# Kernel tuning notes

Hardware: AMD Instinct MI355X
Metric: run time of the kernel (lower is better)

## Reference

```python
import jax, jax.numpy as jnp
import numpy as np

N_NODES = 100000
N_EDGES = 1600000
F_IN, HID = 256, 256
HID_OUT = HID // 2  # last SAGE layer output


def _glorot(key, shape):
    fan_in, fan_out = shape[1], shape[0]
    lim = (6.0 / (fan_in + fan_out)) ** 0.5
    return jax.random.uniform(key, shape, jnp.float32, -lim, lim)


def setup_inputs() -> dict:
    key = jax.random.key(0)
    ks = jax.random.split(key, 12)
    x = jax.random.normal(ks[0], (N_NODES, F_IN), jnp.float32)
    edge_index = jax.random.randint(ks[1], (2, N_EDGES), 0, N_NODES, jnp.int64)
    # SAGEConv params: lin_l (on aggregated neighbors, has bias), lin_r (on root)
    dims = [(F_IN, HID), (HID, HID), (HID, HID_OUT)]
    inp = {"x": x, "edge_index": edge_index}
    for i, (din, dout) in enumerate(dims):
        inp[f"Wl{i}"] = _glorot(ks[2 + 3 * i], (dout, din))
        inp[f"Wr{i}"] = _glorot(ks[3 + 3 * i], (dout, din))
        inp[f"b{i}"] = jnp.zeros((dout,), jnp.float32)
    inp["Wc"] = _glorot(ks[11], (1, HID_OUT))
    inp["bc"] = jnp.zeros((1,), jnp.float32)
    return inp


def _sage_conv(x, src, dst, Wl, Wr, b):
    # mean aggregation of source features at destination nodes
    msg_sum = jax.ops.segment_sum(x[src], dst, num_segments=N_NODES)  # [N, d]
    deg = jax.ops.segment_sum(jnp.ones((src.shape[0], 1), x.dtype), dst,
                              num_segments=N_NODES)  # [N, 1]
    agg = msg_sum / jnp.maximum(deg, 1.0)
    return agg @ Wl.T + x @ Wr.T + b


def reference(x, edge_index, Wl0, Wr0, b0, Wl1, Wr1, b1, Wl2, Wr2, b2, Wc, bc):
    src, dst = edge_index[0], edge_index[1]
    layers = [(Wl0, Wr0, b0), (Wl1, Wr1, b1), (Wl2, Wr2, b2)]
    h = x
    for i, (Wl, Wr, b) in enumerate(layers):
        h = _sage_conv(h, src, dst, Wl, Wr, b)
        if i < len(layers) - 1:
            h = jax.nn.relu(h)  # dropout is identity in eval mode
    return jax.nn.sigmoid(h @ Wc.T + bc)  # [N, 1]
```

## Files before the change

### kernel.cpp

```cpp
#include <hip/hip_runtime.h>
#include <math.h>

#define N_NODES 100000
#define N_PAD   100352
#define N_EDGES 1600000
#define DIN 256

#define NB 782
#define NC 256
#define CHUNK 6250
#define MT_N (NB * NC)
#define MT_PAD 200448

typedef unsigned short u16;
typedef unsigned char u8;
typedef unsigned int u32;
typedef __attribute__((ext_vector_type(8))) short bf16x8;
typedef __attribute__((ext_vector_type(8))) unsigned short us8;
typedef __attribute__((ext_vector_type(4))) float f32x4;
typedef __attribute__((ext_vector_type(2))) float f32x2;

__device__ __forceinline__ float b2f(u16 u) {
    union { unsigned int i; float f; } c; c.i = ((unsigned int)u) << 16; return c.f;
}
__device__ __forceinline__ u16 f2b(float f) {
    union { float f; unsigned int i; } c; c.f = f;
    unsigned int x = c.i;
    return (u16)((x + 0x7fffu + ((x >> 16) & 1u)) >> 16);
}
__device__ __forceinline__ u8 f32_to_fp8(float v) {
    return (u8)(__builtin_amdgcn_cvt_pk_fp8_f32(v, 0.0f, 0, false) & 0xff);
}
__device__ __forceinline__ void accum16(float* a, uint4 v) {
    unsigned int w[4] = { v.x, v.y, v.z, v.w };
    #pragma unroll
    for (int q = 0; q < 4; ++q) {
        f32x2 lo = __builtin_amdgcn_cvt_pk_f32_fp8(w[q], false);
        f32x2 hi = __builtin_amdgcn_cvt_pk_f32_fp8(w[q], true);
        a[q * 4 + 0] += lo[0]; a[q * 4 + 1] += lo[1];
        a[q * 4 + 2] += hi[0]; a[q * 4 + 3] += hi[1];
    }
}
__device__ __forceinline__ void accum8(float* a, uint2 v) {
    unsigned int w[2] = { v.x, v.y };
    #pragma unroll
    for (int q = 0; q < 2; ++q) {
        f32x2 lo = __builtin_amdgcn_cvt_pk_f32_fp8(w[q], false);
        f32x2 hi = __builtin_amdgcn_cvt_pk_f32_fp8(w[q], true);
        a[q * 4 + 0] += lo[0]; a[q * 4 + 1] += lo[1];
        a[q * 4 + 2] += hi[0]; a[q * 4 + 3] += hi[1];
    }
}

__device__ __forceinline__ void gload_lds16(const u16* g, u16* lds_base) {
    __builtin_amdgcn_global_load_lds(
        (const __attribute__((address_space(1))) void*)g,
        (__attribute__((address_space(3))) void*)lds_base, 16, 0, 0);
}

__global__ void cvt_kernel(const float* __restrict__ in, u16* __restrict__ outb,
                           u8* __restrict__ out8, int n4) {
    int i = blockIdx.x * blockDim.x + threadIdx.x;
    if (i < n4) {
        float4 v = ((const float4*)in)[i];
        ushort4 o;
        o.x = f2b(v.x); o.y = f2b(v.y); o.z = f2b(v.z); o.w = f2b(v.w);
        ((ushort4*)outb)[i] = o;
        u32 r = __builtin_amdgcn_cvt_pk_fp8_f32(v.x, v.y, 0, false);
        r = __builtin_amdgcn_cvt_pk_fp8_f32(v.z, v.w, r, true);
        ((u32*)out8)[i] = r;
    }
}

__global__ void cvtw_kernel(const float* __restrict__ Wl0, const float* __restrict__ Wr0,
                            const float* __restrict__ Wl1, const float* __restrict__ Wr1,
                            const float* __restrict__ Wl2, const float* __restrict__ Wr2,
                            u16* __restrict__ wl0, u16* __restrict__ wr0,
                            u16* __restrict__ wl1, u16* __restrict__ wr1,
                            u16* __restrict__ wl2, u16* __restrict__ wr2) {
    int b = blockIdx.x;
    const float* s; u16* d; int i;
    if (b < 64)       { s = Wl0; d = wl0; i = b * 256 + threadIdx.x; }
    else if (b < 128) { s = Wr0; d = wr0; i = (b - 64) * 256 + threadIdx.x; }
    else if (b < 192) { s = Wl1; d = wl1; i = (b - 128) * 256 + threadIdx.x; }
    else if (b < 256) { s = Wr1; d = wr1; i = (b - 192) * 256 + threadIdx.x; }
    else if (b < 288) { s = Wl2; d = wl2; i = (b - 256) * 256 + threadIdx.x; }
    else              { s = Wr2; d = wr2; i = (b - 288) * 256 + threadIdx.x; }
    float4 v = ((const float4*)s)[i];
    ushort4 o;
    o.x = f2b(v.x); o.y = f2b(v.y); o.z = f2b(v.z); o.w = f2b(v.w);
    ((ushort4*)d)[i] = o;
}

__launch_bounds__(256)
__global__ void p1_hist(const int* __restrict__ dst, int* __restrict__ MT) {
    __shared__ int bins[NB];
    const int c = blockIdx.x, tid = threadIdx.x;
    for (int b = tid; b < NB; b += 256) bins[b] = 0;
    __syncthreads();
    const int e0 = c * CHUNK;
    for (int e = e0 + tid; e < e0 + CHUNK; e += 256)
        atomicAdd(&bins[dst[e] >> 7], 1);
    __syncthreads();
    for (int b = tid; b < NB; b += 256) MT[b * NC + c] = bins[b];
}

__global__ void scan1_kernel(const int* __restrict__ in, int* __restrict__ excl,
                             int* __restrict__ blocksums, int n) {
    __shared__ int s[256];
    int tid = threadIdx.x;
    int i = blockIdx.x * 256 + tid;
    int v = (i < n) ? in[i] : 0;
    s[tid] = v;
    __syncthreads();
    for (int off = 1; off < 256; off <<= 1) {
        int t = (tid >= off) ? s[tid - off] : 0;
        __syncthreads();
        s[tid] += t;
        __syncthreads();
    }
    if (i < n) excl[i] = s[tid] - v;
    if (tid == 255) blocksums[blockIdx.x] = s[255];
}

__global__ void scan_carry_kernel(int* __restrict__ bsums, int nb) {
    __shared__ int s[256];
    int tid = threadIdx.x;
    int carry = 0;
    for (int base = 0; base < nb; base += 256) {
        int i = base + tid;
        int v = (i < nb) ? bsums[i] : 0;
        s[tid] = v;
        __syncthreads();
        for (int off = 1; off < 256; off <<= 1) {
            int t = (tid >= off) ? s[tid - off] : 0;
            __syncthreads();
            s[tid] += t;
            __syncthreads();
        }
        int incl = s[tid];
        int tot = s[255];
        if (i < nb) bsums[i] = incl - v + carry;
        carry += tot;
        __syncthreads();
    }
}

__global__ void scan3_kernel(int* __restrict__ excl, const int* __restrict__ blocksums, int n) {
    int i = blockIdx.x * 256 + threadIdx.x;
    if (i < n) excl[i] += blocksums[blockIdx.x];
}

__launch_bounds__(256)
__global__ void p2_partition(const int* __restrict__ src, const int* __restrict__ dst,
                             const int* __restrict__ scanMT, u32* __restrict__ csr_tmp) {
    __shared__ int cur[NB];
    const int c = blockIdx.x, tid = threadIdx.x;
    for (int b = tid; b < NB; b += 256) cur[b] = scanMT[b * NC + c];
    __syncthreads();
    const int e0 = c * CHUNK;
    for (int e = e0 + tid; e < e0 + CHUNK; e += 256) {
        int d = dst[e];
        int pos = atomicAdd(&cur[d >> 7], 1);
        csr_tmp[pos] = ((u32)(d & 127) << 25) | (u32)src[e];
    }
}

__launch_bounds__(256)
__global__ void p3_csr(const int* __restrict__ scanMT, const u32* __restrict__ csr_tmp,
                       int* __restrict__ csr, int* __restrict__ rowptr,
                       int* __restrict__ rowend, float* __restrict__ rinv) {
    __shared__ int cnt[128];
    __shared__ int excl[128];
    __shared__ int cur[128];
    const int b = blockIdx.x, tid = threadIdx.x;
    const int beg = scanMT[b * NC];
    const int end = (b == NB - 1) ? N_EDGES : scanMT[(b + 1) * NC];
    if (tid < 128) cnt[tid] = 0;
    __syncthreads();
    for (int e = beg + tid; e < end; e += 256)
        atomicAdd(&cnt[csr_tmp[e] >> 25], 1);
    __syncthreads();
    if (tid == 0) {
        int run = 0;
        for (int i = 0; i < 128; ++i) { excl[i] = run; run += cnt[i]; }
    }
    __syncthreads();
    if (tid < 128) cur[tid] = beg + excl[tid];
    __syncthreads();
    for (int e = beg + tid; e < end; e += 256) {
        u32 v = csr_tmp[e];
        int pos = atomicAdd(&cur[v >> 25], 1);
        csr[pos] = (int)(v & 0x1FFFFFFu);
    }
    if (tid < 128) {
        int node = b * 128 + tid;
        if (node < N_NODES) {
            int rp = beg + excl[tid];
            rowptr[node] = rp;
            rowend[node] = rp + cnt[tid];
            rinv[node]   = 1.0f / (float)max(cnt[tid], 1);
        }
    }
}

__launch_bounds__(256)
__global__ void agg_kernel(const int* __restrict__ rowptr, const int* __restrict__ rowend,
                           const int* __restrict__ csr_src, const float* __restrict__ rinv,
                           const u8* __restrict__ h8, u16* __restrict__ agg) {
    int node = blockIdx.x * 16 + (threadIdx.x >> 4);
    int lane = threadIdx.x & 15;
    if (node >= N_NODES) return;
    int beg = rowptr[node];
    int end = rowend[node];
    const u8* hl = h8 + lane * 16;
    float a[16] = {};
    int p = beg;
    for (; p + 3 < end; p += 4) {
        int s0 = csr_src[p], s1 = csr_src[p + 1], s2 = csr_src[p + 2], s3 = csr_src[p + 3];
        uint4 v0 = *(const uint4*)(hl + (size_t)s0 * 256);
        uint4 v1 = *(const uint4*)(hl + (size_t)s1 * 256);
        uint4 v2 = *(const uint4*)(hl + (size_t)s2 * 256);
        uint4 v3 = *(const uint4*)(hl + (size_t)s3 * 256);
        accum16(a, v0); accum16(a, v1); accum16(a, v2); accum16(a, v3);
    }
    for (; p < end; ++p) {
        uint4 v0 = *(const uint4*)(hl + (size_t)csr_src[p] * 256);
        accum16(a, v0);
    }
    float r = rinv[node];
    us8 o0, o1;
    #pragma unroll
    for (int j = 0; j < 8; ++j) { o0[j] = f2b(a[j] * r); o1[j] = f2b(a[8 + j] * r); }
    u16* d = agg + (size_t)node * DIN + lane * 16;
    *(us8*)d = o0;
    *(us8*)(d + 8) = o1;
}

template <int MODE>
__launch_bounds__(256)
__global__ void sage_gemm(const u16* __restrict__ A0, const u16* __restrict__ A1,
                          const u16* __restrict__ B0w, const u16* __restrict__ B1w,
                          const float* __restrict__ bias, void* __restrict__ out0,
                          void* __restrict__ out1, u8* __restrict__ out8,
                          int dout, int do_relu) {
    __shared__ u16 sA[2][128 * 32];
    __shared__ u16 sB[2][128 * 32];

    const int t    = threadIdx.x;
    const int row0 = blockIdx.x * 128;
    const int col0 = (MODE == 0) ? blockIdx.y * 128 : 0;
    const int w    = t >> 6, lane = t & 63;
    const int wr   = w >> 1, wc = w & 1;
    const int lr   = lane & 15, lg = lane >> 4;
    const int srow = lane >> 2;
    const int sblk = (lane & 3) ^ (srow & 3);
    const u16* Bsrc_all = (MODE == 1 && blockIdx.y == 1) ? B1w : B0w;

    f32x4 acc[4][4] = {};
    const int NT = (MODE == 0) ? 16 : 8;

    auto stage = [&](int buf, int tk) {
        const int kt = tk * 32;
        const u16* Asrc = (MODE == 0 && kt >= 256) ? A1 : A0;
        const u16* Bsrc = (MODE == 0) ? ((kt >= 256) ? B1w : B0w) : Bsrc_all;
        const int  kb   = (MODE == 0 && kt >= 256) ? kt - 256 : kt;
        #pragma unroll
        for (int i = 0; i < 2; ++i) {
            int row = w * 32 + i * 16 + srow;
            gload_lds16(Asrc + (size_t)(row0 + row) * DIN + kb + sblk * 8,
                        &sA[buf][w * 1024 + i * 512]);
            gload_lds16(Bsrc + (size_t)(col0 + row) * DIN + kb + sblk * 8,
                        &sB[buf][w * 1024 + i * 512]);
        }
    };

    stage(0, 0);
    __syncthreads();
    for (int tk = 0; tk < NT; ++tk) {
        const int cur = tk & 1;
        if (tk + 1 < NT) stage(cur ^ 1, tk + 1);
        bf16x8 af[4], bfr[4];
        #pragma unroll
        for (int m = 0; m < 4; ++m) {
            int row = wr * 64 + m * 16 + lr;
            af[m] = *(const bf16x8*)&sA[cur][row * 32 + 8 * (lg ^ (lr & 3))];
        }
        #pragma unroll
        for (int n = 0; n < 4; ++n) {
            int row = wc * 64 + n * 16 + lr;
            bfr[n] = *(const bf16x8*)&sB[cur][row * 32 + 8 * (lg ^ (lr & 3))];
        }
        #pragma unroll
        for (int m = 0; m < 4; ++m)
            #pragma unroll
            for (int n = 0; n < 4; ++n)
                acc[m][n] = __builtin_amdgcn_mfma_f32_16x16x32_bf16(af[m], bfr[n], acc[m][n], 0, 0, 0);
        __syncthreads();
    }

    const bool f32out = (MODE == 1) && (blockIdx.y == 1);
    #pragma unroll
    for (int m = 0; m < 4; ++m) {
        int row = row0 + wr * 64 + m * 16 + lg * 4;
        #pragma unroll
        for (int n = 0; n < 4; ++n) {
            int col = col0 + wc * 64 + n * 16 + lr;
            #pragma unroll
            for (int r = 0; r < 4; ++r) {
                float v = acc[m][n][r];
                if (MODE == 0) {
                    v += bias[col];
                    if (do_relu) v = fmaxf(v, 0.0f);
                    ((u16*)out0)[(size_t)(row + r) * dout + col] = f2b(v);
                    if (out8) out8[(size_t)(row + r) * dout + col] = f32_to_fp8(v);
                } else if (f32out) {
                    v += bias[col];
                    ((float*)out1)[(size_t)(row + r) * dout + col] = v;
                } else {
                    out8[(size_t)(row + r) * dout + col] = f32_to_fp8(v);
                }
            }
        }
    }
}

__launch_bounds__(256)
__global__ void aggcls_kernel(const int* __restrict__ rowptr, const int* __restrict__ rowend,
                              const int* __restrict__ csr_src, const float* __restrict__ rinv,
                              const u8* __restrict__ z28, const float* __restrict__ y2,
                              const float* __restrict__ Wc, const float* __restrict__ bc,
                              float* __restrict__ out) {
    __shared__ float sW[128];
    int t = threadIdx.x;
    if (t < 128) sW[t] = Wc[t];
    __syncthreads();
    int node = blockIdx.x * 16 + (t >> 4);
    int lane = t & 15;
    if (node >= N_NODES) return;
    int beg = rowptr[node];
    int end = rowend[node];
    const u8* zl = z28 + lane * 8;
    float a[8] = {};
    int p = beg;
    for (; p + 3 < end; p += 4) {
        int s0 = csr_src[p], s1 = csr_src[p + 1], s2 = csr_src[p + 2], s3 = csr_src[p + 3];
        uint2 v0 = *(const uint2*)(zl + (size_t)s0 * 128);
        uint2 v1 = *(const uint2*)(zl + (size_t)s1 * 128);
        uint2 v2 = *(const uint2*)(zl + (size_t)s2 * 128);
        uint2 v3 = *(const uint2*)(zl + (size_t)s3 * 128);
        accum8(a, v0); accum8(a, v1); accum8(a, v2); accum8(a, v3);
    }
    for (; p < end; ++p) {
        uint2 v0 = *(const uint2*)(zl + (size_t)csr_src[p] * 128);
        accum8(a, v0);
    }
    float r = rinv[node];
    float4 ylo = *(const float4*)(y2 + (size_t)node * 128 + lane * 8);
    float4 yhi = *(const float4*)(y2 + (size_t)node * 128 + lane * 8 + 4);
    float yv[8] = { ylo.x, ylo.y, ylo.z, ylo.w, yhi.x, yhi.y, yhi.z, yhi.w };
    float s = 0.f;
    #pragma unroll
    for (int j = 0; j < 8; ++j)
        s += (a[j] * r + yv[j]) * sW[lane * 8 + j];
    #pragma unroll
    for (int off = 8; off; off >>= 1) s += __shfl_xor(s, off, 16);
    if (lane == 0) {
        float z = s + bc[0];
        out[node] = 1.0f / (1.0f + expf(-z));
    }
}

extern "C" void kernel_launch(void* const* d_in, const int* in_sizes, int n_in,
                              void* d_out, int out_size, void* d_ws, size_t ws_size,
                              hipStream_t stream) {
    const float* x   = (const float*)d_in[0];
    const int*   ei  = (const int*)d_in[1];
    const float* Wl0 = (const float*)d_in[2];
    const float* Wr0 = (const float*)d_in[3];
    const float* b0  = (const float*)d_in[4];
    const float* Wl1 = (const float*)d_in[5];
    const float* Wr1 = (const float*)d_in[6];
    const float* b1  = (const float*)d_in[7];
    const float* Wl2 = (const float*)d_in[8];
    const float* Wr2 = (const float*)d_in[9];
    const float* b2  = (const float*)d_in[10];
    const float* Wc  = (const float*)d_in[11];
    const float* bc  = (const float*)d_in[12];
    float* out = (float*)d_out;

    const int* src = ei;
    const int* dst = ei + N_EDGES;

    int*   MT     = (int*)d_ws;
    int*   MTs    = MT + MT_PAD;
    int*   bsums  = MTs + MT_PAD;
    u32*   csrtmp = (u32*)(bsums + 1024);
    int*   csr    = (int*)(csrtmp + N_EDGES);
    int*   rowptr = csr + N_EDGES;
    int*   rowend = rowptr + N_PAD;
    float* rinv   = (float*)(rowend + N_PAD);
    u16*   xb     = (u16*)(rinv + N_PAD);
    u16*   wb     = xb + (size_t)N_PAD * 256;
    u16*   bufA   = wb + 327680;
    u16*   bufB   = bufA + (size_t)N_PAD * 256;
    u16*   bufC   = bufB + (size_t)N_PAD * 256;
    u8*    x8     = (u8*)(bufC + (size_t)N_PAD * 256);
    u8*    h18    = x8 + (size_t)N_PAD * 256;
    u8*    z28    = h18 + (size_t)N_PAD * 256;

    u16* wl0 = wb;
    u16* wr0 = wl0 + 65536;
    u16* wl1 = wr0 + 65536;
    u16* wr1 = wl1 + 65536;
    u16* wl2 = wr1 + 65536;
    u16* wr2 = wl2 + 32768;

    cvt_kernel<<<(N_NODES * 64 + 255) / 256, 256, 0, stream>>>(x, xb, x8, N_NODES * 64);
    cvtw_kernel<<<320, 256, 0, stream>>>(Wl0, Wr0, Wl1, Wr1, Wl2, Wr2,
                                         wl0, wr0, wl1, wr1, wl2, wr2);

    const int scan_blocks = (MT_N + 255) / 256;
    p1_hist<<<NC, 256, 0, stream>>>(dst, MT);
    scan1_kernel<<<scan_blocks, 256, 0, stream>>>(MT, MTs, bsums, MT_N);
    scan_carry_kernel<<<1, 256, 0, stream>>>(bsums, scan_blocks);
    scan3_kernel<<<scan_blocks, 256, 0, stream>>>(MTs, bsums, MT_N);
    p2_partition<<<NC, 256, 0, stream>>>(src, dst, MTs, csrtmp);
    p3_csr<<<NB, 256, 0, stream>>>(MTs, csrtmp, csr, rowptr, rowend, rinv);

    const int Mblocks = (N_NODES + 127) / 128;
    dim3 g01(Mblocks, 2);
    dim3 g2(Mblocks, 2);
    const int agg_blocks = (N_NODES + 15) / 16;

    agg_kernel<<<agg_blocks, 256, 0, stream>>>(rowptr, rowend, csr, rinv, x8, bufA);
    sage_gemm<0><<<g01, 256, 0, stream>>>(bufA, xb, wl0, wr0, b0, bufB, nullptr, h18, 256, 1);

    agg_kernel<<<agg_blocks, 256, 0, stream>>>(rowptr, rowend, csr, rinv, h18, bufA);
    sage_gemm<0><<<g01, 256, 0, stream>>>(bufA, bufB, wl1, wr1, b1, bufC, nullptr, nullptr, 256, 1);

    sage_gemm<1><<<g2, 256, 0, stream>>>(bufC, nullptr, wl2, wr2, b2, nullptr, bufB, z28, 128, 0);
    aggcls_kernel<<<agg_blocks, 256, 0, stream>>>(rowptr, rowend, csr, rinv,
                                                  z28, (const float*)bufB, Wc, bc, out);
}
```

Before: 435.4 us.

## Remap GEMM blocks per XCD, deepen LDS prefetch, and change swizzle pattern

The 2D GEMM grid becomes a 1D grid. Block ids are remapped so consecutive tiles, including both column halves of a row tile, land on the same XCD, which should improve L2 reuse of the A rows. The K loop now issues loads two stages ahead, using explicit vmcnt waits and raw barriers in place of __syncthreads, so global-to-LDS loads overlap the MFMA work. The LDS XOR swizzle is also changed to a different bit pattern to reduce bank conflicts. The manual waitcnt and barrier scheme is fragile if the compiler reorders or the count of outstanding loads differs from the assumed four.

```diff
diff --git a/kernel.cpp b/kernel.cpp
--- a/kernel.cpp
+++ b/kernel.cpp
@@ -56,6 +56,13 @@
     __builtin_amdgcn_global_load_lds(
         (const __attribute__((address_space(1))) void*)g,
         (__attribute__((address_space(3))) void*)lds_base, 16, 0, 0);
+}
+
+__device__ __forceinline__ u32 xcd_chunk(u32 orig, u32 nwg) {
+    u32 q = nwg >> 3, r = nwg & 7;
+    u32 xcd = orig & 7, idx = orig >> 3;
+    u32 base = (xcd < r) ? xcd * (q + 1) : r * (q + 1) + (xcd - r) * q;
+    return base + idx;
 }
 
 __global__ void cvt_kernel(const float* __restrict__ in, u16* __restrict__ outb,
@@ -247,15 +254,17 @@
     __shared__ u16 sA[2][128 * 32];
     __shared__ u16 sB[2][128 * 32];
 
+    const u32 u    = xcd_chunk(blockIdx.x, gridDim.x);
+    const int csel = u & 1;
+    const int row0 = (int)(u >> 1) * 128;
+    const int col0 = (MODE == 0) ? csel * 128 : 0;
     const int t    = threadIdx.x;
-    const int row0 = blockIdx.x * 128;
-    const int col0 = (MODE == 0) ? blockIdx.y * 128 : 0;
     const int w    = t >> 6, lane = t & 63;
     const int wr   = w >> 1, wc = w & 1;
     const int lr   = lane & 15, lg = lane >> 4;
     const int srow = lane >> 2;
-    const int sblk = (lane & 3) ^ (srow & 3);
-    const u16* Bsrc_all = (MODE == 1 && blockIdx.y == 1) ? B1w : B0w;
+    const int sblk = (lane & 3) ^ ((lane >> 3) & 3);
+    const u16* Bsel = csel ? B1w : B0w;
 
     f32x4 acc[4][4] = {};
     const int NT = (MODE == 0) ? 16 : 8;
@@ -263,7 +272,7 @@
     auto stage = [&](int buf, int tk) {
         const int kt = tk * 32;
         const u16* Asrc = (MODE == 0 && kt >= 256) ? A1 : A0;
-        const u16* Bsrc = (MODE == 0) ? ((kt >= 256) ? B1w : B0w) : Bsrc_all;
+        const u16* Bsrc = (MODE == 0) ? ((kt >= 256) ? B1w : B0w) : Bsel;
         const int  kb   = (MODE == 0 && kt >= 256) ? kt - 256 : kt;
         #pragma unroll
         for (int i = 0; i < 2; ++i) {
@@ -276,30 +285,38 @@
     };
 
     stage(0, 0);
-    __syncthreads();
+    stage(1, 1);
     for (int tk = 0; tk < NT; ++tk) {
         const int cur = tk & 1;
-        if (tk + 1 < NT) stage(cur ^ 1, tk + 1);
+        if (tk + 1 < NT) asm volatile("s_waitcnt vmcnt(4)" ::: "memory");
+        else             asm volatile("s_waitcnt vmcnt(0)" ::: "memory");
+        __builtin_amdgcn_sched_barrier(0);
+        __builtin_amdgcn_s_barrier();
+
         bf16x8 af[4], bfr[4];
         #pragma unroll
         for (int m = 0; m < 4; ++m) {
             int row = wr * 64 + m * 16 + lr;
-            af[m] = *(const bf16x8*)&sA[cur][row * 32 + 8 * (lg ^ (lr & 3))];
+            af[m] = *(const bf16x8*)&sA[cur][row * 32 + 8 * (lg ^ ((lr >> 1) & 3))];
         }
         #pragma unroll
         for (int n = 0; n < 4; ++n) {
             int row = wc * 64 + n * 16 + lr;
-            bfr[n] = *(const bf16x8*)&sB[cur][row * 32 + 8 * (lg ^ (lr & 3))];
+            bfr[n] = *(const bf16x8*)&sB[cur][row * 32 + 8 * (lg ^ ((lr >> 1) & 3))];
         }
         #pragma unroll
         for (int m = 0; m < 4; ++m)
             #pragma unroll
             for (int n = 0; n < 4; ++n)
                 acc[m][n] = __builtin_amdgcn_mfma_f32_16x16x32_bf16(af[m], bfr[n], acc[m][n], 0, 0, 0);
-        __syncthreads();
-    }
-
-    const bool f32out = (MODE == 1) && (blockIdx.y == 1);
+
+        asm volatile("s_waitcnt lgkmcnt(0)" ::: "memory");
+        __builtin_amdgcn_sched_barrier(0);
+        __builtin_amdgcn_s_barrier();
+        if (tk + 2 < NT) stage(cur, tk + 2);
+    }
+
+    const bool f32out = (MODE == 1) && (csel == 1);
     #pragma unroll
     for (int m = 0; m < 4; ++m) {
         int row = row0 + wr * 64 + m * 16 + lg * 4;
@@ -429,17 +446,16 @@
     p3_csr<<<NB, 256, 0, stream>>>(MTs, csrtmp, csr, rowptr, rowend, rinv);
 
     const int Mblocks = (N_NODES + 127) / 128;
-    dim3 g01(Mblocks, 2);
-    dim3 g2(Mblocks, 2);
+    const int gemm_blocks = Mblocks * 2;
     const int agg_blocks = (N_NODES + 15) / 16;
 
     agg_kernel<<<agg_blocks, 256, 0, stream>>>(rowptr, rowend, csr, rinv, x8, bufA);
-    sage_gemm<0><<<g01, 256, 0, stream>>>(bufA, xb, wl0, wr0, b0, bufB, nullptr, h18, 256, 1);
+    sage_gemm<0><<<gemm_blocks, 256, 0, stream>>>(bufA, xb, wl0, wr0, b0, bufB, nullptr, h18, 256, 1);
 
     agg_kernel<<<agg_blocks, 256, 0, stream>>>(rowptr, rowend, csr, rinv, h18, bufA);
-    sage_gemm<0><<<g01, 256, 0, stream>>>(bufA, bufB, wl1, wr1, b1, bufC, nullptr, nullptr, 256, 1);
-
-    sage_gemm<1><<<g2, 256, 0, stream>>>(bufC, nullptr, wl2, wr2, b2, nullptr, bufB, z28, 128, 0);
+    sage_gemm<0><<<gemm_blocks, 256, 0, stream>>>(bufA, bufB, wl1, wr1, b1, bufC, nullptr, nullptr, 256, 1);
+
+    sage_gemm<1><<<gemm_blocks, 256, 0, stream>>>(bufC, nullptr, wl2, wr2, b2, nullptr, bufB, z28, 128, 0);
     aggcls_kernel<<<agg_blocks, 256, 0, stream>>>(rowptr, rowend, csr, rinv,
                                                   z28, (const float*)bufB, Wc, bc, out);
 }
```

After: 421.9 us. -3.1%, faster.
